# Optimization experiments

Measured on AMD Instinct MI355X. Metric: run time of the kernel, lower is better.

Reference implementation:

```python
import jax, jax.numpy as jnp
import numpy as np

N = 50000      # nodes
E = 500000     # edges
D_IN = 512
D_H = 512
D_OUT = 256


def setup_inputs() -> dict:
    key = jax.random.key(0)
    ks = jax.random.split(key, 5)
    x = jax.random.normal(ks[0], (N, D_IN), dtype=jnp.float32)
    edge_index = jax.random.randint(ks[1], (2, E), 0, N, dtype=jnp.int32)
    W1 = jax.random.normal(ks[2], (D_IN, D_H), dtype=jnp.float32) / np.float32(np.sqrt(D_IN))
    b1 = jnp.zeros((D_H,), dtype=jnp.float32)
    W2 = jax.random.normal(ks[3], (D_H, D_OUT), dtype=jnp.float32) / np.float32(np.sqrt(D_H))
    b2 = jnp.zeros((D_OUT,), dtype=jnp.float32)
    return {"x": x, "edge_index": edge_index, "W1": W1, "b1": b1, "W2": W2, "b2": b2}


def _gcn_conv(x, src, dst, W, b, n):
    # PyG GCNConv: h = X W; add self-loops; symmetric norm D^-1/2 (A+I) D^-1/2; aggregate at dst; + bias
    h = x @ W
    loop = jnp.arange(n, dtype=src.dtype)
    src_sl = jnp.concatenate([src, loop])
    dst_sl = jnp.concatenate([dst, loop])
    deg = jax.ops.segment_sum(jnp.ones_like(src_sl, dtype=h.dtype), dst_sl, num_segments=n)
    dinv = jnp.where(deg > 0, jax.lax.rsqrt(deg), 0.0)
    norm = dinv[src_sl] * dinv[dst_sl]                     # [E+N]
    msg = h[src_sl] * norm[:, None]                        # [E+N, out]
    out = jax.ops.segment_sum(msg, dst_sl, num_segments=n) # [N, out]
    return out + b


def reference(x, edge_index, W1, b1, W2, b2):
    # Encoder.forward in eval mode (dropout = identity, bn='none' = identity), ELU activation after each conv.
    src, dst = edge_index[0], edge_index[1]
    h = _gcn_conv(x, src, dst, W1, b1, N)
    h = jax.nn.elu(h)
    h = _gcn_conv(h, src, dst, W2, b2, N)
    return jax.nn.elu(h)
```

## Files before the change

kernel.cpp:

```cpp
#include <hip/hip_runtime.h>
#include <math.h>

#define N_NODES 50000
#define N_EDGES 500000
#define D_IN 512
#define D_H  512
#define D_OUT 256
#define NB 196

typedef __attribute__((ext_vector_type(8))) short bf16x8;
typedef __attribute__((ext_vector_type(8))) unsigned short ushort8;
typedef __attribute__((ext_vector_type(4))) float f32x4;

__device__ __forceinline__ float b2f(unsigned short u) {
    union { unsigned int i; float f; } v; v.i = ((unsigned int)u) << 16; return v.f;
}
__device__ __forceinline__ unsigned short f2b(float f) {
    unsigned int x = __float_as_uint(f);
    unsigned int r = (x + 0x7fffu + ((x >> 16) & 1u)) >> 16;
    return (unsigned short)r;
}


#define ZB   196
#define CB   12500
#define W1B  256
#define W2B  128

__global__ __launch_bounds__(256) void k_prep(const float* __restrict__ x,
                                              unsigned short* __restrict__ xb,
                                              const float* __restrict__ W1,
                                              unsigned short* __restrict__ W1t,
                                              const float* __restrict__ W2,
                                              unsigned short* __restrict__ W2t,
                                              int* __restrict__ indeg) {
    __shared__ float t[32][33];
    const int b = blockIdx.x;
    const int tid = threadIdx.x;

    if (b < ZB) {
        const int i = b * 256 + tid;
        if (i < N_NODES) indeg[i] = 0;
        return;
    }
    if (b < ZB + CB) {
        const long long i = (long long)(b - ZB) * 256 + tid;
        float4 v0 = ((const float4*)x)[i * 2];
        float4 v1 = ((const float4*)x)[i * 2 + 1];
        ushort8 o;
        o[0] = f2b(v0.x); o[1] = f2b(v0.y); o[2] = f2b(v0.z); o[3] = f2b(v0.w);
        o[4] = f2b(v1.x); o[5] = f2b(v1.y); o[6] = f2b(v1.z); o[7] = f2b(v1.w);
        ((ushort8*)xb)[i] = o;
        return;
    }
    const float* W;
    unsigned short* Wt;
    int K, N, idx;
    if (b < ZB + CB + W1B) {
        W = W1; Wt = W1t; K = D_IN; N = D_H; idx = b - (ZB + CB);
    } else {
        W = W2; Wt = W2t; K = D_H; N = D_OUT; idx = b - (ZB + CB + W1B);
    }
    const int nkb = K / 32;
    const int bk = (idx % nkb) * 32;
    const int bn = (idx / nkb) * 32;
    const int tx = tid & 31, ty = tid >> 5;
    for (int i = ty; i < 32; i += 8) t[i][tx] = W[(size_t)(bk + i) * N + bn + tx];
    __syncthreads();
    for (int i = ty; i < 32; i += 8)
        Wt[(size_t)(bn + i) * K + bk + tx] = f2b(t[tx][i]);
}


__global__ __launch_bounds__(256) void k_indeg(const int* __restrict__ dst,
                                               int* __restrict__ indeg) {
    int i = blockIdx.x * 256 + threadIdx.x;
    if (i < N_EDGES) atomicAdd(&indeg[dst[i]], 1);
}

__global__ __launch_bounds__(256) void k_partials(const int* __restrict__ indeg,
                                                  int* __restrict__ bsum) {
    __shared__ int wsum[4];
    const int tid = threadIdx.x, lane = tid & 63, w = tid >> 6;
    const int i = blockIdx.x * 256 + tid;
    int v = (i < N_NODES) ? indeg[i] : 0;
#pragma unroll
    for (int o = 32; o > 0; o >>= 1) v += __shfl_down(v, o, 64);
    if (lane == 0) wsum[w] = v;
    __syncthreads();
    if (tid == 0) bsum[blockIdx.x] = wsum[0] + wsum[1] + wsum[2] + wsum[3];
}

__global__ __launch_bounds__(256) void k_scanb(const int* __restrict__ bsum,
                                               int* __restrict__ boff) {
    __shared__ int wsum[4];
    const int tid = threadIdx.x, lane = tid & 63, w = tid >> 6;
    const int v = (tid < NB) ? bsum[tid] : 0;
    int s = v;
#pragma unroll
    for (int o = 1; o < 64; o <<= 1) {
        int t = __shfl_up(s, o, 64);
        if (lane >= o) s += t;
    }
    if (lane == 63) wsum[w] = s;
    __syncthreads();
    int add = 0;
    for (int k = 0; k < w; ++k) add += wsum[k];
    if (tid < NB) boff[tid] = add + s - v;
}

__global__ __launch_bounds__(256) void k_finalize(const int* __restrict__ indeg,
                                                  const int* __restrict__ boff,
                                                  int* __restrict__ row_start,
                                                  int* __restrict__ cursor,
                                                  float* __restrict__ dinv) {
    __shared__ int wsum[4];
    const int tid = threadIdx.x, lane = tid & 63, w = tid >> 6;
    const int i = blockIdx.x * 256 + tid;
    const int v = (i < N_NODES) ? indeg[i] : 0;
    int s = v;
#pragma unroll
    for (int o = 1; o < 64; o <<= 1) {
        int t = __shfl_up(s, o, 64);
        if (lane >= o) s += t;
    }
    if (lane == 63) wsum[w] = s;
    __syncthreads();
    int add = boff[blockIdx.x];
    for (int k = 0; k < w; ++k) add += wsum[k];
    if (i < N_NODES) {
        const int excl = add + s - v;
        row_start[i] = excl;
        cursor[i] = excl;
        dinv[i] = rsqrtf((float)(1 + v));
    }
    if (i == N_NODES) row_start[N_NODES] = N_EDGES;
}

__global__ __launch_bounds__(256) void k_bucket(const int* __restrict__ src,
                                                const int* __restrict__ dst,
                                                int* __restrict__ cursor,
                                                int* __restrict__ csr_src) {
    int e = blockIdx.x * 256 + threadIdx.x;
    if (e >= N_EDGES) return;
    int pos = atomicAdd(&cursor[dst[e]], 1);
    csr_src[pos] = src[e];
}


__device__ __forceinline__ void gload16(const void* g, void* l) {
    __builtin_amdgcn_global_load_lds(
        (const __attribute__((address_space(1))) unsigned int*)g,
        (__attribute__((address_space(3))) unsigned int*)l, 16, 0, 0);
}

__global__ __launch_bounds__(256, 2) void k_gemm(const unsigned short* __restrict__ A,
                                                 const unsigned short* __restrict__ Bt,
                                                 unsigned short* __restrict__ C,
                                                 int M, int N, int K,
                                                 int ncb, int nrb) {
    __shared__ __align__(16) short As[2][128 * 64];
    __shared__ __align__(16) short Bs[2][128 * 64];

    const int bid = blockIdx.x;
    const int xcd = bid & 7;
    const int sidx = bid >> 3;
    const int cb = sidx % ncb;
    const int rb = (sidx / ncb) * 8 + xcd;
    if (rb >= nrb) return;
    const int brow = rb * 128;
    const int bcol = cb * 128;

    const int tid = threadIdx.x;
    const int wid = tid >> 6;
    const int lane = tid & 63;
    const int wr = wid >> 1, wc = wid & 1;
    const int lhi = lane >> 4, llo = lane & 15;

    f32x4 acc[4][4];
#pragma unroll
    for (int i = 0; i < 4; ++i)
#pragma unroll
        for (int j = 0; j < 4; ++j) acc[i][j] = (f32x4){0.f, 0.f, 0.f, 0.f};

#define STAGE(buf, kt)                                                          \
    {                                                                           \
        _Pragma("unroll") for (int g = 0; g < 4; ++g) {                         \
            const int s = g * 256 + tid;                                        \
            const int row = s >> 3;                                             \
            const int sc = (s & 7) ^ (row & 7);                                 \
            int gr = brow + row; gr = gr < M ? gr : M - 1;                      \
            gload16(A + (size_t)gr * K + (kt) + sc * 8,                         \
                    &As[buf][(g * 256 + wid * 64) * 8]);                        \
            gload16(Bt + (size_t)(bcol + row) * K + (kt) + sc * 8,              \
                    &Bs[buf][(g * 256 + wid * 64) * 8]);                        \
        }                                                                       \
    }

    const int nt = K / 64;

    STAGE(0, 0);
    __syncthreads();

    int cur = 0;
    for (int t = 0; t < nt; ++t) {
        if (t + 1 < nt) STAGE(cur ^ 1, (t + 1) * 64);

#pragma unroll
        for (int ks = 0; ks < 2; ++ks) {
            bf16x8 af[4], bf[4];
#pragma unroll
            for (int mi = 0; mi < 4; ++mi) {
                const int row = wr * 64 + mi * 16 + llo;
                af[mi] = *(const bf16x8*)&As[cur][row * 64 + (((ks * 4 + lhi) ^ (llo & 7)) * 8)];
            }
#pragma unroll
            for (int ni = 0; ni < 4; ++ni) {
                const int row = wc * 64 + ni * 16 + llo;
                bf[ni] = *(const bf16x8*)&Bs[cur][row * 64 + (((ks * 4 + lhi) ^ (llo & 7)) * 8)];
            }
#pragma unroll
            for (int mi = 0; mi < 4; ++mi)
#pragma unroll
                for (int ni = 0; ni < 4; ++ni)
                    acc[mi][ni] = __builtin_amdgcn_mfma_f32_16x16x32_bf16(
                        af[mi], bf[ni], acc[mi][ni], 0, 0, 0);
        }

        __syncthreads();
        cur ^= 1;
    }
#undef STAGE

    short* cws = &As[0][0] + wid * 4096;

#pragma unroll
    for (int mi = 0; mi < 4; ++mi)
#pragma unroll
        for (int ni = 0; ni < 4; ++ni) {
            const f32x4 v = acc[mi][ni];
#pragma unroll
            for (int r = 0; r < 4; ++r) {
                const int row = mi * 16 + lhi * 4 + r;
                const int col = ni * 16 + llo;
                const int chunk = (col >> 3) ^ (row & 7);
                cws[row * 64 + chunk * 8 + (col & 7)] = (short)f2b(v[r]);
            }
        }
    __syncthreads();

    {
        const int rsub = lane >> 3;
        const int c = lane & 7;
#pragma unroll
        for (int i = 0; i < 8; ++i) {
            const int row = i * 8 + rsub;
            const ushort8 o = *(const ushort8*)&cws[row * 64 + ((c ^ (row & 7)) * 8)];
            const int grow = brow + wr * 64 + row;
            if (grow < M)
                *(ushort8*)(C + (size_t)grow * N + bcol + wc * 64 + c * 8) = o;
        }
    }
}


template <int D, bool BF16_OUT>
__global__ __launch_bounds__(256) void k_aggregate(const unsigned short* __restrict__ H,
                                                   const float* __restrict__ bias,
                                                   void* __restrict__ outv,
                                                   const int* __restrict__ row_start,
                                                   const int* __restrict__ csr_src,
                                                   const float* __restrict__ dinv) {
    const int wid = threadIdx.x >> 6;
    const int lane = threadIdx.x & 63;
    int n, c0;
    if (D == 512) { n = blockIdx.x * 4 + wid; c0 = lane * 8; }
    else          { n = blockIdx.x * 8 + wid * 2 + (lane >> 5); c0 = (lane & 31) * 8; }
    if (n >= N_NODES) return;

    const float di = dinv[n];
    float acc[8];
    {
        const float ws = di * di;
        ushort8 v = *(const ushort8*)(H + (size_t)n * D + c0);
#pragma unroll
        for (int e = 0; e < 8; ++e) acc[e] = b2f(v[e]) * ws;
    }

    const int e0 = row_start[n];
    const int e1 = row_start[n + 1];
    int j = e0;
    for (; j + 8 <= e1; j += 8) {
        int s[8];
        float wgt[8];
#pragma unroll
        for (int q = 0; q < 8; ++q) s[q] = csr_src[j + q];
#pragma unroll
        for (int q = 0; q < 8; ++q) wgt[q] = dinv[s[q]] * di;
#pragma unroll
        for (int h = 0; h < 2; ++h) {
            const ushort8 v0 = *(const ushort8*)(H + (size_t)s[h * 4 + 0] * D + c0);
            const ushort8 v1 = *(const ushort8*)(H + (size_t)s[h * 4 + 1] * D + c0);
            const ushort8 v2 = *(const ushort8*)(H + (size_t)s[h * 4 + 2] * D + c0);
            const ushort8 v3 = *(const ushort8*)(H + (size_t)s[h * 4 + 3] * D + c0);
#pragma unroll
            for (int e = 0; e < 8; ++e) {
                acc[e] = fmaf(b2f(v0[e]), wgt[h * 4 + 0], acc[e]);
                acc[e] = fmaf(b2f(v1[e]), wgt[h * 4 + 1], acc[e]);
                acc[e] = fmaf(b2f(v2[e]), wgt[h * 4 + 2], acc[e]);
                acc[e] = fmaf(b2f(v3[e]), wgt[h * 4 + 3], acc[e]);
            }
        }
    }
    for (; j + 4 <= e1; j += 4) {
        const int s0 = csr_src[j + 0];
        const int s1 = csr_src[j + 1];
        const int s2 = csr_src[j + 2];
        const int s3 = csr_src[j + 3];
        const float w0 = dinv[s0] * di;
        const float w1 = dinv[s1] * di;
        const float w2 = dinv[s2] * di;
        const float w3 = dinv[s3] * di;
        const ushort8 v0 = *(const ushort8*)(H + (size_t)s0 * D + c0);
        const ushort8 v1 = *(const ushort8*)(H + (size_t)s1 * D + c0);
        const ushort8 v2 = *(const ushort8*)(H + (size_t)s2 * D + c0);
        const ushort8 v3 = *(const ushort8*)(H + (size_t)s3 * D + c0);
#pragma unroll
        for (int e = 0; e < 8; ++e) {
            acc[e] = fmaf(b2f(v0[e]), w0, acc[e]);
            acc[e] = fmaf(b2f(v1[e]), w1, acc[e]);
            acc[e] = fmaf(b2f(v2[e]), w2, acc[e]);
            acc[e] = fmaf(b2f(v3[e]), w3, acc[e]);
        }
    }
    for (; j < e1; ++j) {
        const int s = csr_src[j];
        const float ws = dinv[s] * di;
        const ushort8 v = *(const ushort8*)(H + (size_t)s * D + c0);
#pragma unroll
        for (int e = 0; e < 8; ++e) acc[e] = fmaf(b2f(v[e]), ws, acc[e]);
    }

#pragma unroll
    for (int e = 0; e < 8; ++e) {
        float t = acc[e] + bias[c0 + e];
        acc[e] = t > 0.f ? t : expf(t) - 1.f;
    }

    if (BF16_OUT) {
        ushort8 o;
#pragma unroll
        for (int e = 0; e < 8; ++e) o[e] = f2b(acc[e]);
        *(ushort8*)((unsigned short*)outv + (size_t)n * D + c0) = o;
    } else {
        float* orow = (float*)outv + (size_t)n * D + c0;
        *(float4*)orow = make_float4(acc[0], acc[1], acc[2], acc[3]);
        *(float4*)(orow + 4) = make_float4(acc[4], acc[5], acc[6], acc[7]);
    }
}


extern "C" void kernel_launch(void* const* d_in, const int* in_sizes, int n_in,
                              void* d_out, int out_size, void* d_ws, size_t ws_size,
                              hipStream_t stream) {
    const float* x  = (const float*)d_in[0];
    const int* ei   = (const int*)d_in[1];
    const int* src  = ei;
    const int* dst  = ei + N_EDGES;
    const float* W1 = (const float*)d_in[2];
    const float* b1 = (const float*)d_in[3];
    const float* W2 = (const float*)d_in[4];
    const float* b2 = (const float*)d_in[5];
    float* out = (float*)d_out;

    char* ws = (char*)d_ws;
    size_t off = 0;
    auto alloc = [&](size_t bytes) -> void* {
        void* p = ws + off;
        off = (off + bytes + 255) & ~(size_t)255;
        return p;
    };
    int*   indeg     = (int*)alloc((size_t)N_NODES * 4);
    int*   bsum      = (int*)alloc((size_t)NB * 4);
    int*   boff      = (int*)alloc((size_t)NB * 4);
    int*   row_start = (int*)alloc((size_t)(N_NODES + 1) * 4);
    int*   cursor    = (int*)alloc((size_t)N_NODES * 4);
    int*   csr_src   = (int*)alloc((size_t)N_EDGES * 4);
    float* dinv      = (float*)alloc((size_t)N_NODES * 4);
    unsigned short* W1t  = (unsigned short*)alloc((size_t)D_H * D_IN * 2);
    unsigned short* W2t  = (unsigned short*)alloc((size_t)D_OUT * D_H * 2);
    unsigned short* xb   = (unsigned short*)alloc((size_t)N_NODES * D_IN * 2);
    unsigned short* H1   = (unsigned short*)alloc((size_t)N_NODES * D_H * 2);
    unsigned short* out1 = (unsigned short*)alloc((size_t)N_NODES * D_H * 2);
    unsigned short* H2   = (unsigned short*)alloc((size_t)N_NODES * D_OUT * 2);

    k_prep<<<ZB + CB + W1B + W2B, 256, 0, stream>>>(x, xb, W1, W1t, W2, W2t, indeg);

    k_indeg<<<(N_EDGES + 255) / 256, 256, 0, stream>>>(dst, indeg);
    k_partials<<<NB, 256, 0, stream>>>(indeg, bsum);
    k_scanb<<<1, 256, 0, stream>>>(bsum, boff);
    k_finalize<<<NB, 256, 0, stream>>>(indeg, boff, row_start, cursor, dinv);
    k_bucket<<<(N_EDGES + 255) / 256, 256, 0, stream>>>(src, dst, cursor, csr_src);

    const int nrb = (N_NODES + 127) / 128;
    const int rgrp = (nrb + 7) / 8;

    {
        const int ncb = D_H / 128;
        k_gemm<<<8 * ncb * rgrp, 256, 0, stream>>>(xb, W1t, H1, N_NODES, D_H, D_IN, ncb, nrb);
    }
    k_aggregate<512, true><<<(N_NODES + 3) / 4, 256, 0, stream>>>(H1, b1, out1, row_start, csr_src, dinv);

    {
        const int ncb = D_OUT / 128;
        k_gemm<<<8 * ncb * rgrp, 256, 0, stream>>>(out1, W2t, H2, N_NODES, D_OUT, D_H, ncb, nrb);
    }
    k_aggregate<256, false><<<(N_NODES + 7) / 8, 256, 0, stream>>>(H2, b2, out, row_start, csr_src, dinv);
}
```

Measured before the change: 284.0 us.

## Fold source-degree scaling into GEMM epilogue and fuse CSR build into launches

Each GEMM epilogue now multiplies every output row by dinv of that row, so the aggregation does plain sums and applies the destination dinv once at the end. This drops the per-edge dinv gather and multiply. The in-degree atomics move into the prep kernel and the CSR bucket fill moves into extra blocks of the first GEMM, which removes separate launches. The cost is one extra zeroing kernel and a rounding change, since rows are scaled before the bf16 cast.

```diff
diff --git a/kernel.cpp b/kernel.cpp
--- a/kernel.cpp
+++ b/kernel.cpp
@@ -7,6 +7,7 @@
 #define D_H  512
 #define D_OUT 256
 #define NB 196
+#define NBK 1954
 
 typedef __attribute__((ext_vector_type(8))) short bf16x8;
 typedef __attribute__((ext_vector_type(8))) unsigned short ushort8;
@@ -22,7 +23,12 @@
 }
 
 
-#define ZB   196
+__global__ __launch_bounds__(256) void k_zero(int* __restrict__ p, int n) {
+    int i = blockIdx.x * 256 + threadIdx.x;
+    if (i < n) p[i] = 0;
+}
+
+
 #define CB   12500
 #define W1B  256
 #define W2B  128
@@ -33,18 +39,20 @@
                                               unsigned short* __restrict__ W1t,
                                               const float* __restrict__ W2,
                                               unsigned short* __restrict__ W2t,
+                                              const int* __restrict__ dst,
                                               int* __restrict__ indeg) {
     __shared__ float t[32][33];
-    const int b = blockIdx.x;
+    int b = blockIdx.x;
     const int tid = threadIdx.x;
 
-    if (b < ZB) {
-        const int i = b * 256 + tid;
-        if (i < N_NODES) indeg[i] = 0;
+    if (b < NBK) {
+        const int e = b * 256 + tid;
+        if (e < N_EDGES) atomicAdd(&indeg[dst[e]], 1);
         return;
     }
-    if (b < ZB + CB) {
-        const long long i = (long long)(b - ZB) * 256 + tid;
+    b -= NBK;
+    if (b < CB) {
+        const long long i = (long long)b * 256 + tid;
         float4 v0 = ((const float4*)x)[i * 2];
         float4 v1 = ((const float4*)x)[i * 2 + 1];
         ushort8 o;
@@ -53,14 +61,12 @@
         ((ushort8*)xb)[i] = o;
         return;
     }
+    b -= CB;
     const float* W;
     unsigned short* Wt;
     int K, N, idx;
-    if (b < ZB + CB + W1B) {
-        W = W1; Wt = W1t; K = D_IN; N = D_H; idx = b - (ZB + CB);
-    } else {
-        W = W2; Wt = W2t; K = D_H; N = D_OUT; idx = b - (ZB + CB + W1B);
-    }
+    if (b < W1B) { W = W1; Wt = W1t; K = D_IN; N = D_H; idx = b; }
+    else         { W = W2; Wt = W2t; K = D_H; N = D_OUT; idx = b - W1B; }
     const int nkb = K / 32;
     const int bk = (idx % nkb) * 32;
     const int bn = (idx / nkb) * 32;
@@ -71,12 +77,6 @@
         Wt[(size_t)(bn + i) * K + bk + tx] = f2b(t[tx][i]);
 }
 
-
-__global__ __launch_bounds__(256) void k_indeg(const int* __restrict__ dst,
-                                               int* __restrict__ indeg) {
-    int i = blockIdx.x * 256 + threadIdx.x;
-    if (i < N_EDGES) atomicAdd(&indeg[dst[i]], 1);
-}
 
 __global__ __launch_bounds__(256) void k_partials(const int* __restrict__ indeg,
                                                   int* __restrict__ bsum) {
@@ -137,16 +137,6 @@
     if (i == N_NODES) row_start[N_NODES] = N_EDGES;
 }
 
-__global__ __launch_bounds__(256) void k_bucket(const int* __restrict__ src,
-                                                const int* __restrict__ dst,
-                                                int* __restrict__ cursor,
-                                                int* __restrict__ csr_src) {
-    int e = blockIdx.x * 256 + threadIdx.x;
-    if (e >= N_EDGES) return;
-    int pos = atomicAdd(&cursor[dst[e]], 1);
-    csr_src[pos] = src[e];
-}
-
 
 __device__ __forceinline__ void gload16(const void* g, void* l) {
     __builtin_amdgcn_global_load_lds(
@@ -154,15 +144,29 @@
         (__attribute__((address_space(3))) unsigned int*)l, 16, 0, 0);
 }
 
+template <bool FUSE_BUCKET>
 __global__ __launch_bounds__(256, 2) void k_gemm(const unsigned short* __restrict__ A,
                                                  const unsigned short* __restrict__ Bt,
                                                  unsigned short* __restrict__ C,
+                                                 const float* __restrict__ rowscale,
                                                  int M, int N, int K,
-                                                 int ncb, int nrb) {
+                                                 int ncb, int nrb,
+                                                 const int* __restrict__ src,
+                                                 const int* __restrict__ dst,
+                                                 int* __restrict__ cursor,
+                                                 int* __restrict__ csr_src) {
     __shared__ __align__(16) short As[2][128 * 64];
     __shared__ __align__(16) short Bs[2][128 * 64];
 
-    const int bid = blockIdx.x;
+    if (FUSE_BUCKET && blockIdx.x < NBK) {
+        const int e = blockIdx.x * 256 + threadIdx.x;
+        if (e < N_EDGES) {
+            const int pos = atomicAdd(&cursor[dst[e]], 1);
+            csr_src[pos] = src[e];
+        }
+        return;
+    }
+    const int bid = blockIdx.x - (FUSE_BUCKET ? NBK : 0);
     const int xcd = bid & 7;
     const int sidx = bid >> 3;
     const int cb = sidx % ncb;
@@ -235,18 +239,21 @@
     short* cws = &As[0][0] + wid * 4096;
 
 #pragma unroll
-    for (int mi = 0; mi < 4; ++mi)
-#pragma unroll
-        for (int ni = 0; ni < 4; ++ni) {
-            const f32x4 v = acc[mi][ni];
-#pragma unroll
-            for (int r = 0; r < 4; ++r) {
-                const int row = mi * 16 + lhi * 4 + r;
+    for (int mi = 0; mi < 4; ++mi) {
+#pragma unroll
+        for (int r = 0; r < 4; ++r) {
+            const int lrow = mi * 16 + lhi * 4 + r;
+            int grow = brow + wr * 64 + lrow;
+            grow = grow < M ? grow : M - 1;
+            const float ds = rowscale[grow];
+#pragma unroll
+            for (int ni = 0; ni < 4; ++ni) {
                 const int col = ni * 16 + llo;
-                const int chunk = (col >> 3) ^ (row & 7);
-                cws[row * 64 + chunk * 8 + (col & 7)] = (short)f2b(v[r]);
+                const int chunk = (col >> 3) ^ (lrow & 7);
+                cws[lrow * 64 + chunk * 8 + (col & 7)] = (short)f2b(acc[mi][ni][r] * ds);
             }
         }
+    }
     __syncthreads();
 
     {
@@ -278,13 +285,11 @@
     else          { n = blockIdx.x * 8 + wid * 2 + (lane >> 5); c0 = (lane & 31) * 8; }
     if (n >= N_NODES) return;
 
-    const float di = dinv[n];
     float acc[8];
     {
-        const float ws = di * di;
         ushort8 v = *(const ushort8*)(H + (size_t)n * D + c0);
 #pragma unroll
-        for (int e = 0; e < 8; ++e) acc[e] = b2f(v[e]) * ws;
+        for (int e = 0; e < 8; ++e) acc[e] = b2f(v[e]);
     }
 
     const int e0 = row_start[n];
@@ -292,11 +297,8 @@
     int j = e0;
     for (; j + 8 <= e1; j += 8) {
         int s[8];
-        float wgt[8];
 #pragma unroll
         for (int q = 0; q < 8; ++q) s[q] = csr_src[j + q];
-#pragma unroll
-        for (int q = 0; q < 8; ++q) wgt[q] = dinv[s[q]] * di;
 #pragma unroll
         for (int h = 0; h < 2; ++h) {
             const ushort8 v0 = *(const ushort8*)(H + (size_t)s[h * 4 + 0] * D + c0);
@@ -305,10 +307,10 @@
             const ushort8 v3 = *(const ushort8*)(H + (size_t)s[h * 4 + 3] * D + c0);
 #pragma unroll
             for (int e = 0; e < 8; ++e) {
-                acc[e] = fmaf(b2f(v0[e]), wgt[h * 4 + 0], acc[e]);
-                acc[e] = fmaf(b2f(v1[e]), wgt[h * 4 + 1], acc[e]);
-                acc[e] = fmaf(b2f(v2[e]), wgt[h * 4 + 2], acc[e]);
-                acc[e] = fmaf(b2f(v3[e]), wgt[h * 4 + 3], acc[e]);
+                acc[e] += b2f(v0[e]);
+                acc[e] += b2f(v1[e]);
+                acc[e] += b2f(v2[e]);
+                acc[e] += b2f(v3[e]);
             }
         }
     }
@@ -317,33 +319,29 @@
         const int s1 = csr_src[j + 1];
         const int s2 = csr_src[j + 2];
         const int s3 = csr_src[j + 3];
-        const float w0 = dinv[s0] * di;
-        const float w1 = dinv[s1] * di;
-        const float w2 = dinv[s2] * di;
-        const float w3 = dinv[s3] * di;
         const ushort8 v0 = *(const ushort8*)(H + (size_t)s0 * D + c0);
         const ushort8 v1 = *(const ushort8*)(H + (size_t)s1 * D + c0);
         const ushort8 v2 = *(const ushort8*)(H + (size_t)s2 * D + c0);
         const ushort8 v3 = *(const ushort8*)(H + (size_t)s3 * D + c0);
 #pragma unroll
         for (int e = 0; e < 8; ++e) {
-            acc[e] = fmaf(b2f(v0[e]), w0, acc[e]);
-            acc[e] = fmaf(b2f(v1[e]), w1, acc[e]);
-            acc[e] = fmaf(b2f(v2[e]), w2, acc[e]);
-            acc[e] = fmaf(b2f(v3[e]), w3, acc[e]);
+            acc[e] += b2f(v0[e]);
+            acc[e] += b2f(v1[e]);
+            acc[e] += b2f(v2[e]);
+            acc[e] += b2f(v3[e]);
         }
     }
     for (; j < e1; ++j) {
         const int s = csr_src[j];
-        const float ws = dinv[s] * di;
         const ushort8 v = *(const ushort8*)(H + (size_t)s * D + c0);
 #pragma unroll
-        for (int e = 0; e < 8; ++e) acc[e] = fmaf(b2f(v[e]), ws, acc[e]);
-    }
-
+        for (int e = 0; e < 8; ++e) acc[e] += b2f(v[e]);
+    }
+
+    const float di = dinv[n];
 #pragma unroll
     for (int e = 0; e < 8; ++e) {
-        float t = acc[e] + bias[c0 + e];
+        float t = fmaf(acc[e], di, bias[c0 + e]);
         acc[e] = t > 0.f ? t : expf(t) - 1.f;
     }
 
@@ -394,26 +392,26 @@
     unsigned short* out1 = (unsigned short*)alloc((size_t)N_NODES * D_H * 2);
     unsigned short* H2   = (unsigned short*)alloc((size_t)N_NODES * D_OUT * 2);
 
-    k_prep<<<ZB + CB + W1B + W2B, 256, 0, stream>>>(x, xb, W1, W1t, W2, W2t, indeg);
-
-    k_indeg<<<(N_EDGES + 255) / 256, 256, 0, stream>>>(dst, indeg);
+    k_zero<<<NB, 256, 0, stream>>>(indeg, N_NODES);
+    k_prep<<<NBK + CB + W1B + W2B, 256, 0, stream>>>(x, xb, W1, W1t, W2, W2t, dst, indeg);
     k_partials<<<NB, 256, 0, stream>>>(indeg, bsum);
     k_scanb<<<1, 256, 0, stream>>>(bsum, boff);
     k_finalize<<<NB, 256, 0, stream>>>(indeg, boff, row_start, cursor, dinv);
-    k_bucket<<<(N_EDGES + 255) / 256, 256, 0, stream>>>(src, dst, cursor, csr_src);
 
     const int nrb = (N_NODES + 127) / 128;
     const int rgrp = (nrb + 7) / 8;
 
     {
         const int ncb = D_H / 128;
-        k_gemm<<<8 * ncb * rgrp, 256, 0, stream>>>(xb, W1t, H1, N_NODES, D_H, D_IN, ncb, nrb);
+        k_gemm<true><<<NBK + 8 * ncb * rgrp, 256, 0, stream>>>(
+            xb, W1t, H1, dinv, N_NODES, D_H, D_IN, ncb, nrb, src, dst, cursor, csr_src);
     }
     k_aggregate<512, true><<<(N_NODES + 3) / 4, 256, 0, stream>>>(H1, b1, out1, row_start, csr_src, dinv);
 
     {
         const int ncb = D_OUT / 128;
-        k_gemm<<<8 * ncb * rgrp, 256, 0, stream>>>(out1, W2t, H2, N_NODES, D_OUT, D_H, ncb, nrb);
+        k_gemm<false><<<8 * ncb * rgrp, 256, 0, stream>>>(
+            out1, W2t, H2, dinv, N_NODES, D_OUT, D_H, ncb, nrb, nullptr, nullptr, nullptr, nullptr);
     }
     k_aggregate<256, false><<<(N_NODES + 7) / 8, 256, 0, stream>>>(H2, b2, out, row_start, csr_src, dinv);
 }
```

Measured after the change: 275.1 us. 3.1% less time.
